# Performance work log

Measured on AMD Instinct MI355X. Metric: run time of the kernel, lower is better.

Reference implementation:

```python
import jax, jax.numpy as jnp
import numpy as np
import math

N_HEAD = 16
D_MODEL = 1024
ATT_DIM = D_MODEL // N_HEAD


def setup_inputs() -> dict:
    key = jax.random.key(0)
    ks = jax.random.split(key, 11)
    B, T, D = 2, 2048, D_MODEL
    s = 1.0 / math.sqrt(D)
    return {
        "q": jax.random.normal(ks[0], (B, T, D), jnp.float32),
        "k": jax.random.normal(ks[1], (B, T, D), jnp.float32),
        "v": jax.random.normal(ks[2], (B, T, D), jnp.float32),
        "Wq": jax.random.normal(ks[3], (D, D), jnp.float32) * s,
        "bq": jnp.zeros((D,), jnp.float32),
        "Wk": jax.random.normal(ks[4], (D, D), jnp.float32) * s,
        "bk": jnp.zeros((D,), jnp.float32),
        "Wv": jax.random.normal(ks[5], (D, D), jnp.float32) * s,
        "bv": jnp.zeros((D,), jnp.float32),
        "Wo": jax.random.normal(ks[6], (D, D), jnp.float32) * s,
        "bo": jnp.zeros((D,), jnp.float32),
    }


def reference(q, k, v, Wq, bq, Wk, bk, Wv, bv, Wo, bo):
    B, T, D = q.shape
    H, hd = N_HEAD, ATT_DIM
    # Linear projections (torch Linear: x @ W.T + b)
    qh = (q @ Wq.T + bq).reshape(B, T, H, hd).transpose(0, 2, 1, 3)  # [B,H,T,hd]
    kh = (k @ Wk.T + bk).reshape(B, T, H, hd).transpose(0, 2, 1, 3)
    vh = (v @ Wv.T + bv).reshape(B, T, H, hd).transpose(0, 2, 1, 3)
    scale = 1.0 / math.sqrt(hd)
    score = jnp.einsum("bhqd,bhkd->bhqk", qh, kh) * scale  # [B,H,T,T]
    attn = jax.nn.softmax(score, axis=-1)
    out = jnp.einsum("bhqk,bhkd->bhqd", attn, vh)  # [B,H,T,hd]
    out = out.transpose(0, 2, 1, 3).reshape(B, T, D)
    return out @ Wo.T + bo
```

## Files before the change

kernel.cpp:

```cpp
#include <hip/hip_runtime.h>


typedef __attribute__((ext_vector_type(8))) short bf16x8;
typedef __attribute__((ext_vector_type(4))) float f32x4;

#define E22 ((size_t)1 << 22)
#define E20 ((size_t)1 << 20)

__device__ __forceinline__ unsigned short f2bf(float x) {
    unsigned int u = __float_as_uint(x);
    u += 0x7fffu + ((u >> 16) & 1u);
    return (unsigned short)(u >> 16);
}
__device__ __forceinline__ unsigned int pk2bf(float a, float b) {
    return __builtin_amdgcn_perm(__float_as_uint(a), __float_as_uint(b), 0x03020706u);
}
__device__ __forceinline__ void gl16(const void* g, void* l) {
    __builtin_amdgcn_global_load_lds(
        (const __attribute__((address_space(1))) void*)g,
        (__attribute__((address_space(3))) void*)l, 16, 0, 0);
}
__device__ __forceinline__ f32x4 mfma16(bf16x8 a, bf16x8 b, f32x4 c) {
    return __builtin_amdgcn_mfma_f32_16x16x32_bf16(a, b, c, 0, 0, 0);
}

__global__ __launch_bounds__(256)
void split_all(const float* __restrict__ q, const float* __restrict__ k,
               const float* __restrict__ v, const float* __restrict__ wq,
               const float* __restrict__ wk, const float* __restrict__ wv,
               const float* __restrict__ wo, unsigned short* __restrict__ ws)
{
    const size_t t = (size_t)blockIdx.x * 256 + threadIdx.x;
    const size_t e = t * 4;
    const float* src; unsigned short* dst; size_t off;
    if (e < 3 * E22) {
        const unsigned int which = (unsigned int)(e >> 22);
        src = which == 0 ? q : (which == 1 ? k : v);
        off = e & (E22 - 1);
        dst = ws + (size_t)which * E22;
    } else {
        const size_t e2 = e - 3 * E22;
        const unsigned int which = (unsigned int)(e2 >> 20);
        off = e2 & (E20 - 1);
        src = which == 0 ? wq : (which == 1 ? wk : (which == 2 ? wv : wo));
        dst = ws + 3 * E22 + (size_t)which * E20;
    }
    const float4 xv = *(const float4*)(src + off);
    ushort4 h4;
    h4.x = f2bf(xv.x); h4.y = f2bf(xv.y); h4.z = f2bf(xv.z); h4.w = f2bf(xv.w);
    *(ushort4*)(dst + off) = h4;
}

__global__ __launch_bounds__(256)
void gemm_qkv(const unsigned short* __restrict__ Xall,
              const unsigned short* __restrict__ Wcat,
              const float* __restrict__ bq, const float* __restrict__ bk,
              const float* __restrict__ bv, unsigned short* __restrict__ Qhp,
              unsigned short* __restrict__ Khp, unsigned short* __restrict__ Vtp)
{
    __shared__ unsigned short Xs[4096], Ws[4096];
    const int tid = threadIdx.x;
    const int w = tid >> 6, ln = tid & 63;
    const int quad = ln >> 4, L = ln & 15;
    const int wy = w >> 1, wx = w & 1;

    const int bid = blockIdx.x;
    const int xcd = bid & 7, j = bid >> 3;
    const int gg = xcd * 12 + (j >> 3);
    const int which = gg >> 5, m_i = gg & 31, n_i = j & 7;
    const int m0 = m_i * 128;

    const unsigned short* X = Xall + (size_t)which * E22;
    const unsigned short* W = Wcat + ((size_t)which * 1024 + n_i * 128) * 1024;
    const float* bp = which == 0 ? bq : (which == 1 ? bk : bv);
    unsigned short* outp = which == 0 ? Qhp : (which == 1 ? Khp : Vtp);
    const float qscale = which == 0 ? 0.18033688011f : 1.0f;

    f32x4 acc[4][4];
#pragma unroll
    for (int i = 0; i < 4; ++i)
#pragma unroll
        for (int jj = 0; jj < 4; ++jj) { f32x4 z = {0.f,0.f,0.f,0.f}; acc[i][jj] = z; }

    for (int k0 = 0; k0 < 1024; k0 += 32) {
        __syncthreads();
#pragma unroll
        for (int i = 0; i < 2; ++i) {
            const int ci  = i * 64 + ln;
            const int row = w * 32 + (ci >> 2);
            const int gc  = (ci & 3) ^ ((row >> 1) & 3);
            const size_t goff = (size_t)row * 1024 + k0 + gc * 8;
            const int lb = w * 2048 + i * 1024;
            gl16(X + (size_t)m0 * 1024 + goff, (char*)Xs + lb);
            gl16(W + goff, (char*)Ws + lb);
        }
        __syncthreads();

        bf16x8 ah[4], bh[4];
#pragma unroll
        for (int mt = 0; mt < 4; ++mt) {
            const int row = wy * 64 + mt * 16 + L;
            ah[mt] = *(const bf16x8*)(Xs + row * 32 + ((quad ^ ((row >> 1) & 3)) * 8));
        }
#pragma unroll
        for (int nt = 0; nt < 4; ++nt) {
            const int row = wx * 64 + nt * 16 + L;
            bh[nt] = *(const bf16x8*)(Ws + row * 32 + ((quad ^ ((row >> 1) & 3)) * 8));
        }
#pragma unroll
        for (int mt = 0; mt < 4; ++mt)
#pragma unroll
            for (int nt = 0; nt < 4; ++nt)
                acc[mt][nt] = mfma16(ah[mt], bh[nt], acc[mt][nt]);
    }

#pragma unroll
    for (int mt = 0; mt < 4; ++mt)
#pragma unroll
        for (int nt = 0; nt < 4; ++nt) {
            const int gm0 = m0 + wy * 64 + mt * 16 + quad * 4;
            const int bn  = n_i * 128 + wx * 64 + nt * 16 + L;
            const float bvv = bp[bn];
            const int hh = bn >> 6, dd = bn & 63;
            if (which < 2) {
#pragma unroll
                for (int r = 0; r < 4; ++r) {
                    const int gm = gm0 + r;
                    const int bb = gm >> 11, tt = gm & 2047;
                    outp[((size_t)(bb * 16 + hh) * 2048 + tt) * 64 + dd] =
                        f2bf((acc[mt][nt][r] + bvv) * qscale);
                }
            } else {
                const int bb = gm0 >> 11, t0 = gm0 & 2047;
                ushort4 pk;
                pk.x = f2bf(acc[mt][nt][0] + bvv);
                pk.y = f2bf(acc[mt][nt][1] + bvv);
                pk.z = f2bf(acc[mt][nt][2] + bvv);
                pk.w = f2bf(acc[mt][nt][3] + bvv);
                *(ushort4*)(outp + ((size_t)(bb * 16 + hh) * 64 + dd) * 2048 + t0) = pk;
            }
        }
}

__global__ __launch_bounds__(256)
void gemm_out(const unsigned short* __restrict__ X, const unsigned short* __restrict__ W,
              const float* __restrict__ bias, float* __restrict__ outp)
{
    __shared__ unsigned short Xs[4096], Ws[2048];
    const int tid = threadIdx.x;
    const int w = tid >> 6, ln = tid & 63;
    const int quad = ln >> 4, L = ln & 15;

    const int bid = blockIdx.x;
    const int xcd = bid & 7, j = bid >> 3;
    const int m0 = (xcd * 4 + (j >> 4)) * 128;
    const int n0 = (j & 15) * 64;

    f32x4 acc[2][4];
#pragma unroll
    for (int i = 0; i < 2; ++i)
#pragma unroll
        for (int jj = 0; jj < 4; ++jj) { f32x4 z = {0.f,0.f,0.f,0.f}; acc[i][jj] = z; }

    for (int k0 = 0; k0 < 1024; k0 += 32) {
        __syncthreads();
#pragma unroll
        for (int i = 0; i < 2; ++i) {
            const int ci  = i * 64 + ln;
            const int row = w * 32 + (ci >> 2);
            const int gc  = (ci & 3) ^ ((row >> 1) & 3);
            const size_t gx = (size_t)(m0 + row) * 1024 + k0 + gc * 8;
            gl16(X + gx, (char*)Xs + w * 2048 + i * 1024);
        }
        {
            const int row = w * 16 + (ln >> 2);
            const int gc  = (ln & 3) ^ ((row >> 1) & 3);
            const size_t gw = (size_t)(n0 + row) * 1024 + k0 + gc * 8;
            gl16(W + gw, (char*)Ws + w * 1024);
        }
        __syncthreads();

        bf16x8 ah[2], bh[4];
#pragma unroll
        for (int mt = 0; mt < 2; ++mt) {
            const int row = w * 32 + mt * 16 + L;
            ah[mt] = *(const bf16x8*)(Xs + row * 32 + ((quad ^ ((row >> 1) & 3)) * 8));
        }
#pragma unroll
        for (int nt = 0; nt < 4; ++nt) {
            const int row = nt * 16 + L;
            bh[nt] = *(const bf16x8*)(Ws + row * 32 + ((quad ^ ((row >> 1) & 3)) * 8));
        }
#pragma unroll
        for (int mt = 0; mt < 2; ++mt)
#pragma unroll
            for (int nt = 0; nt < 4; ++nt)
                acc[mt][nt] = mfma16(ah[mt], bh[nt], acc[mt][nt]);
    }

#pragma unroll
    for (int mt = 0; mt < 2; ++mt)
#pragma unroll
        for (int nt = 0; nt < 4; ++nt) {
            const int gm0 = m0 + w * 32 + mt * 16 + quad * 4;
            const int gn  = n0 + nt * 16 + L;
            const float bvv = bias[gn];
#pragma unroll
            for (int r = 0; r < 4; ++r)
                outp[(size_t)(gm0 + r) * 1024 + gn] = acc[mt][nt][r] + bvv;
        }
}

__global__ __launch_bounds__(256, 2)
void flash(const unsigned short* __restrict__ Qh, const unsigned short* __restrict__ Kh,
           const unsigned short* __restrict__ Vt, unsigned short* __restrict__ A)
{
    __shared__ unsigned short KVs[16384];
    __shared__ unsigned short PT[4 * 64 * 72];
    const int tid = threadIdx.x;
    const int w = tid >> 6, ln = tid & 63;
    const int quad = ln >> 4, L = ln & 15;
    const int wq = w & 1, wk = w >> 1;

    const int bid = blockIdx.x;
    const int xcd = bid & 7, j = bid >> 3;
    const int bh_i = xcd * 4 + (j & 3);
    const int qt = j >> 2;
    const int b = bh_i >> 4, h = bh_i & 15;

    const unsigned short* Qb = Qh + ((size_t)bh_i * 2048 + qt * 128 + wq * 64) * 64;
    const unsigned short* Kb = Kh + (size_t)bh_i * 2048 * 64;
    const unsigned short* Vb = Vt + (size_t)bh_i * 64 * 2048;

    bf16x8 bq[4][2];
#pragma unroll
    for (int nt = 0; nt < 4; ++nt)
#pragma unroll
        for (int kc = 0; kc < 2; ++kc)
            bq[nt][kc] = *(const bf16x8*)(Qb + (nt * 16 + L) * 64 + kc * 32 + quad * 8);

    const short one_bf = (short)0x3F80;
    bf16x8 bone = {one_bf, one_bf, one_bf, one_bf, one_bf, one_bf, one_bf, one_bf};

    f32x4 o[4][4];
    f32x4 lacc[4];
#pragma unroll
    for (int mtd = 0; mtd < 4; ++mtd)
#pragma unroll
        for (int nt = 0; nt < 4; ++nt) { f32x4 z = {0.f,0.f,0.f,0.f}; o[mtd][nt] = z; }
#pragma unroll
    for (int nt = 0; nt < 4; ++nt) { f32x4 z = {0.f,0.f,0.f,0.f}; lacc[nt] = z; }

    unsigned short* Pw = PT + w * 64 * 72;

    const int ci0 = (w * 2 + 0) * 64 + ln, ci1 = (w * 2 + 1) * 64 + ln;
    const int rr0 = ci0 >> 3, rr1 = ci1 >> 3;
    const int gc0 = (ci0 & 7) ^ (rr0 & 7), gc1 = (ci1 & 7) ^ (rr1 & 7);

#define STAGE(kt_, buf_)                                                        \
    do {                                                                        \
        gl16(Kb + (size_t)((kt_) * 64 + rr0) * 64 + gc0 * 8,                    \
             (char*)KVs + (buf_) * 8192 + (w * 2 + 0) * 1024);                  \
        gl16(Kb + (size_t)((kt_) * 64 + rr1) * 64 + gc1 * 8,                    \
             (char*)KVs + (buf_) * 8192 + (w * 2 + 1) * 1024);                  \
        gl16(Vb + (size_t)rr0 * 2048 + (kt_) * 64 + gc0 * 8,                    \
             (char*)KVs + 16384 + (buf_) * 8192 + (w * 2 + 0) * 1024);          \
        gl16(Vb + (size_t)rr1 * 2048 + (kt_) * 64 + gc1 * 8,                    \
             (char*)KVs + 16384 + (buf_) * 8192 + (w * 2 + 1) * 1024);          \
    } while (0)

    STAGE(0, 0);

    for (int kt = 0; kt < 32; ++kt) {
        const int cur = kt & 1;
        __syncthreads();
        if (kt < 31) STAGE(kt + 1, cur ^ 1);

        const unsigned short* Ksb = KVs + cur * 4096;
        const unsigned short* Vsb = KVs + 8192 + cur * 4096;

        bf16x8 ak[2][2];
#pragma unroll
        for (int mt = 0; mt < 2; ++mt)
#pragma unroll
            for (int kc = 0; kc < 2; ++kc) {
                const int row = wk * 32 + mt * 16 + L;
                ak[mt][kc] = *(const bf16x8*)(Ksb + row * 64 + (((kc * 4 + quad) ^ (L & 7)) * 8));
            }

        f32x4 s[2][4];
#pragma unroll
        for (int mt = 0; mt < 2; ++mt)
#pragma unroll
            for (int nt = 0; nt < 4; ++nt) {
                f32x4 z = {0.f,0.f,0.f,0.f};
                z = mfma16(ak[mt][0], bq[nt][0], z);
                z = mfma16(ak[mt][1], bq[nt][1], z);
                s[mt][nt] = z;
            }

#pragma unroll
        for (int mt = 0; mt < 2; ++mt)
#pragma unroll
            for (int nt = 0; nt < 4; ++nt) {
                const float p0 = __builtin_amdgcn_exp2f(s[mt][nt][0]);
                const float p1 = __builtin_amdgcn_exp2f(s[mt][nt][1]);
                const float p2 = __builtin_amdgcn_exp2f(s[mt][nt][2]);
                const float p3 = __builtin_amdgcn_exp2f(s[mt][nt][3]);
                uint2 pk2;
                pk2.x = pk2bf(p0, p1);
                pk2.y = pk2bf(p2, p3);
                *(uint2*)(Pw + (nt * 16 + L) * 72 + mt * 16 + quad * 4) = pk2;
            }
        asm volatile("s_waitcnt lgkmcnt(0)" ::: "memory");

        bf16x8 av[4], pb[4];
#pragma unroll
        for (int mtd = 0; mtd < 4; ++mtd) {
            const int row = mtd * 16 + L;
            av[mtd] = *(const bf16x8*)(Vsb + row * 64 + (((wk * 4 + quad) ^ (L & 7)) * 8));
        }
#pragma unroll
        for (int nt = 0; nt < 4; ++nt)
            pb[nt] = *(const bf16x8*)(Pw + (nt * 16 + L) * 72 + quad * 8);

#pragma unroll
        for (int mtd = 0; mtd < 4; ++mtd)
#pragma unroll
            for (int nt = 0; nt < 4; ++nt)
                o[mtd][nt] = mfma16(av[mtd], pb[nt], o[mtd][nt]);
#pragma unroll
        for (int nt = 0; nt < 4; ++nt)
            lacc[nt] = mfma16(bone, pb[nt], lacc[nt]);
    }
#undef STAGE

    __syncthreads();
    float* Rb = (float*)KVs;
    float* Lb = (float*)PT;
    if (wk == 1) {
#pragma unroll
        for (int mtd = 0; mtd < 4; ++mtd)
#pragma unroll
            for (int nt = 0; nt < 4; ++nt)
                *(f32x4*)(Rb + wq * 4096 + (mtd * 4 + nt) * 256 + ln * 4) = o[mtd][nt];
#pragma unroll
        for (int nt = 0; nt < 4; ++nt)
            *(f32x4*)(Lb + wq * 1024 + nt * 256 + ln * 4) = lacc[nt];
    }
    __syncthreads();
    if (wk == 0) {
#pragma unroll
        for (int mtd = 0; mtd < 4; ++mtd)
#pragma unroll
            for (int nt = 0; nt < 4; ++nt)
                o[mtd][nt] += *(const f32x4*)(Rb + wq * 4096 + (mtd * 4 + nt) * 256 + ln * 4);
#pragma unroll
        for (int nt = 0; nt < 4; ++nt)
            lacc[nt] += *(const f32x4*)(Lb + wq * 1024 + nt * 256 + ln * 4);

#pragma unroll
        for (int nt = 0; nt < 4; ++nt) {
            const float inv = 1.0f / lacc[nt][0];
            const int qrow = b * 2048 + qt * 128 + wq * 64 + nt * 16 + L;
#pragma unroll
            for (int mtd = 0; mtd < 4; ++mtd) {
                const int d0 = mtd * 16 + quad * 4;
                ushort4 pk;
                pk.x = f2bf(o[mtd][nt][0] * inv);
                pk.y = f2bf(o[mtd][nt][1] * inv);
                pk.z = f2bf(o[mtd][nt][2] * inv);
                pk.w = f2bf(o[mtd][nt][3] * inv);
                *(ushort4*)(A + (size_t)qrow * 1024 + h * 64 + d0) = pk;
            }
        }
    }
}

extern "C" void kernel_launch(void* const* d_in, const int* in_sizes, int n_in,
                              void* d_out, int out_size, void* d_ws, size_t ws_size,
                              hipStream_t stream) {
    const float* q  = (const float*)d_in[0];
    const float* k  = (const float*)d_in[1];
    const float* v  = (const float*)d_in[2];
    const float* Wq = (const float*)d_in[3];
    const float* bq = (const float*)d_in[4];
    const float* Wk = (const float*)d_in[5];
    const float* bk = (const float*)d_in[6];
    const float* Wv = (const float*)d_in[7];
    const float* bv = (const float*)d_in[8];
    const float* Wo = (const float*)d_in[9];
    const float* bo = (const float*)d_in[10];

    unsigned short* W = (unsigned short*)d_ws;
    unsigned short *Xall = W;
    unsigned short *Wcat = W + 3 * E22;
    unsigned short *Wob  = Wcat + 3 * E20;
    unsigned short *Qhp  = W + 4 * E22;
    unsigned short *Khp  = W + 5 * E22;
    unsigned short *Vtp  = W + 6 * E22;
    unsigned short *A    = W;

    split_all<<<16384, 256, 0, stream>>>(q, k, v, Wq, Wk, Wv, Wo, W);

    gemm_qkv<<<768, 256, 0, stream>>>(Xall, Wcat, bq, bk, bv, Qhp, Khp, Vtp);

    flash<<<512, 256, 0, stream>>>(Qhp, Khp, Vtp, A);

    gemm_out<<<512, 256, 0, stream>>>(A, Wob, bo, (float*)d_out);
}
```

Baseline: 225.5 us.

## Triple-buffer LDS loads in QKV and output projection GEMMs

Both projection GEMMs now use a three-stage shared-memory ring. Global-to-LDS loads for tile k+2 are issued before the MFMA work on tile k, and a single barrier per iteration, gated by a vmcnt wait, replaces the previous two. The aim is to hide global load latency behind matrix math and cut synchronisation stalls. The cost is three times the LDS per block, which may reduce occupancy, plus hand-counted vmcnt values that must match the number of loads issued.

```diff
diff --git a/kernel.cpp b/kernel.cpp
--- a/kernel.cpp
+++ b/kernel.cpp
@@ -58,7 +58,7 @@
               const float* __restrict__ bv, unsigned short* __restrict__ Qhp,
               unsigned short* __restrict__ Khp, unsigned short* __restrict__ Vtp)
 {
-    __shared__ unsigned short Xs[4096], Ws[4096];
+    __shared__ unsigned short Xs[3 * 4096], Ws[3 * 4096];
     const int tid = threadIdx.x;
     const int w = tid >> 6, ln = tid & 63;
     const int quad = ln >> 4, L = ln & 15;
@@ -76,43 +76,74 @@
     unsigned short* outp = which == 0 ? Qhp : (which == 1 ? Khp : Vtp);
     const float qscale = which == 0 ? 0.18033688011f : 1.0f;
 
+    const int ci0 = ln, ci1 = 64 + ln;
+    const int row0 = w * 32 + (ci0 >> 2), row1 = w * 32 + (ci1 >> 2);
+    const int gc0 = (ci0 & 3) ^ ((row0 >> 1) & 3);
+    const int gc1 = (ci1 & 3) ^ ((row1 >> 1) & 3);
+    const int lb0 = w * 2048, lb1 = w * 2048 + 1024;
+    const unsigned short* Xbp = X + (size_t)m0 * 1024;
+    const size_t gx0 = (size_t)row0 * 1024 + gc0 * 8;
+    const size_t gx1 = (size_t)row1 * 1024 + gc1 * 8;
+
     f32x4 acc[4][4];
 #pragma unroll
     for (int i = 0; i < 4; ++i)
 #pragma unroll
         for (int jj = 0; jj < 4; ++jj) { f32x4 z = {0.f,0.f,0.f,0.f}; acc[i][jj] = z; }
 
-    for (int k0 = 0; k0 < 1024; k0 += 32) {
-        __syncthreads();
-#pragma unroll
-        for (int i = 0; i < 2; ++i) {
-            const int ci  = i * 64 + ln;
-            const int row = w * 32 + (ci >> 2);
-            const int gc  = (ci & 3) ^ ((row >> 1) & 3);
-            const size_t goff = (size_t)row * 1024 + k0 + gc * 8;
-            const int lb = w * 2048 + i * 1024;
-            gl16(X + (size_t)m0 * 1024 + goff, (char*)Xs + lb);
-            gl16(W + goff, (char*)Ws + lb);
-        }
-        __syncthreads();
-
-        bf16x8 ah[4], bh[4];
-#pragma unroll
-        for (int mt = 0; mt < 4; ++mt) {
-            const int row = wy * 64 + mt * 16 + L;
-            ah[mt] = *(const bf16x8*)(Xs + row * 32 + ((quad ^ ((row >> 1) & 3)) * 8));
-        }
-#pragma unroll
-        for (int nt = 0; nt < 4; ++nt) {
-            const int row = wx * 64 + nt * 16 + L;
-            bh[nt] = *(const bf16x8*)(Ws + row * 32 + ((quad ^ ((row >> 1) & 3)) * 8));
-        }
-#pragma unroll
-        for (int mt = 0; mt < 4; ++mt)
-#pragma unroll
-            for (int nt = 0; nt < 4; ++nt)
-                acc[mt][nt] = mfma16(ah[mt], bh[nt], acc[mt][nt]);
-    }
+#define QSTAGE(k0_, bo_)                                                       \
+    do {                                                                       \
+        gl16(Xbp + gx0 + (k0_), (char*)Xs + (bo_) + lb0);                      \
+        gl16(W   + gx0 + (k0_), (char*)Ws + (bo_) + lb0);                      \
+        gl16(Xbp + gx1 + (k0_), (char*)Xs + (bo_) + lb1);                      \
+        gl16(W   + gx1 + (k0_), (char*)Ws + (bo_) + lb1);                      \
+    } while (0)
+
+#define QCOMP(eo_)                                                             \
+    do {                                                                       \
+        const unsigned short* Xc = Xs + (eo_);                                 \
+        const unsigned short* Wc = Ws + (eo_);                                 \
+        bf16x8 ah[4], bh[4];                                                   \
+        _Pragma("unroll")                                                      \
+        for (int mt = 0; mt < 4; ++mt) {                                       \
+            const int row = wy * 64 + mt * 16 + L;                             \
+            ah[mt] = *(const bf16x8*)(Xc + row * 32 +                          \
+                                      ((quad ^ ((row >> 1) & 3)) * 8));        \
+        }                                                                      \
+        _Pragma("unroll")                                                      \
+        for (int nt = 0; nt < 4; ++nt) {                                       \
+            const int row = wx * 64 + nt * 16 + L;                             \
+            bh[nt] = *(const bf16x8*)(Wc + row * 32 +                          \
+                                      ((quad ^ ((row >> 1) & 3)) * 8));        \
+        }                                                                      \
+        _Pragma("unroll")                                                      \
+        for (int mt = 0; mt < 4; ++mt)                                         \
+            _Pragma("unroll")                                                  \
+            for (int nt = 0; nt < 4; ++nt)                                     \
+                acc[mt][nt] = mfma16(ah[mt], bh[nt], acc[mt][nt]);             \
+    } while (0)
+
+    QSTAGE(0, 0);
+    QSTAGE(32, 8192);
+
+    int cur = 0;
+    for (int kt = 0; kt < 31; ++kt) {
+        asm volatile("s_waitcnt vmcnt(4)" ::: "memory");
+        __builtin_amdgcn_s_barrier();
+        asm volatile("" ::: "memory");
+        if (kt < 30) {
+            int st = cur + 2; if (st >= 3) st -= 3;
+            QSTAGE((kt + 2) * 32, st * 8192);
+        }
+        QCOMP(cur * 4096);
+        cur = (cur == 2) ? 0 : cur + 1;
+    }
+    asm volatile("s_waitcnt vmcnt(0)" ::: "memory");
+    __builtin_amdgcn_s_barrier();
+    asm volatile("" ::: "memory");
+    QCOMP(cur * 4096);
+#undef QSTAGE
+#undef QCOMP
 
 #pragma unroll
     for (int mt = 0; mt < 4; ++mt)
@@ -146,7 +177,7 @@
 void gemm_out(const unsigned short* __restrict__ X, const unsigned short* __restrict__ W,
               const float* __restrict__ bias, float* __restrict__ outp)
 {
-    __shared__ unsigned short Xs[4096], Ws[2048];
+    __shared__ unsigned short Xs[3 * 4096], Ws[3 * 2048];
     const int tid = threadIdx.x;
     const int w = tid >> 6, ln = tid & 63;
     const int quad = ln >> 4, L = ln & 15;
@@ -156,47 +187,74 @@
     const int m0 = (xcd * 4 + (j >> 4)) * 128;
     const int n0 = (j & 15) * 64;
 
+    const int cix0 = ln, cix1 = 64 + ln;
+    const int rowx0 = w * 32 + (cix0 >> 2), rowx1 = w * 32 + (cix1 >> 2);
+    const int gcx0 = (cix0 & 3) ^ ((rowx0 >> 1) & 3);
+    const int gcx1 = (cix1 & 3) ^ ((rowx1 >> 1) & 3);
+    const int roww = w * 16 + (ln >> 2);
+    const int gcw = (ln & 3) ^ ((roww >> 1) & 3);
+    const size_t gxx0 = (size_t)(m0 + rowx0) * 1024 + gcx0 * 8;
+    const size_t gxx1 = (size_t)(m0 + rowx1) * 1024 + gcx1 * 8;
+    const size_t gww  = (size_t)(n0 + roww) * 1024 + gcw * 8;
+
     f32x4 acc[2][4];
 #pragma unroll
     for (int i = 0; i < 2; ++i)
 #pragma unroll
         for (int jj = 0; jj < 4; ++jj) { f32x4 z = {0.f,0.f,0.f,0.f}; acc[i][jj] = z; }
 
-    for (int k0 = 0; k0 < 1024; k0 += 32) {
-        __syncthreads();
-#pragma unroll
-        for (int i = 0; i < 2; ++i) {
-            const int ci  = i * 64 + ln;
-            const int row = w * 32 + (ci >> 2);
-            const int gc  = (ci & 3) ^ ((row >> 1) & 3);
-            const size_t gx = (size_t)(m0 + row) * 1024 + k0 + gc * 8;
-            gl16(X + gx, (char*)Xs + w * 2048 + i * 1024);
-        }
-        {
-            const int row = w * 16 + (ln >> 2);
-            const int gc  = (ln & 3) ^ ((row >> 1) & 3);
-            const size_t gw = (size_t)(n0 + row) * 1024 + k0 + gc * 8;
-            gl16(W + gw, (char*)Ws + w * 1024);
-        }
-        __syncthreads();
-
-        bf16x8 ah[2], bh[4];
-#pragma unroll
-        for (int mt = 0; mt < 2; ++mt) {
-            const int row = w * 32 + mt * 16 + L;
-            ah[mt] = *(const bf16x8*)(Xs + row * 32 + ((quad ^ ((row >> 1) & 3)) * 8));
-        }
-#pragma unroll
-        for (int nt = 0; nt < 4; ++nt) {
-            const int row = nt * 16 + L;
-            bh[nt] = *(const bf16x8*)(Ws + row * 32 + ((quad ^ ((row >> 1) & 3)) * 8));
-        }
-#pragma unroll
-        for (int mt = 0; mt < 2; ++mt)
-#pragma unroll
-            for (int nt = 0; nt < 4; ++nt)
-                acc[mt][nt] = mfma16(ah[mt], bh[nt], acc[mt][nt]);
-    }
+#define OSTAGE(k0_, bf_)                                                       \
+    do {                                                                       \
+        gl16(X + gxx0 + (k0_), (char*)Xs + (bf_) * 8192 + w * 2048);           \
+        gl16(X + gxx1 + (k0_), (char*)Xs + (bf_) * 8192 + w * 2048 + 1024);    \
+        gl16(W + gww  + (k0_), (char*)Ws + (bf_) * 4096 + w * 1024);           \
+    } while (0)
+
+#define OCOMP(bf_)                                                             \
+    do {                                                                       \
+        const unsigned short* Xc = Xs + (bf_) * 4096;                          \
+        const unsigned short* Wc = Ws + (bf_) * 2048;                          \
+        bf16x8 ah[2], bh[4];                                                   \
+        _Pragma("unroll")                                                      \
+        for (int mt = 0; mt < 2; ++mt) {                                       \
+            const int row = w * 32 + mt * 16 + L;                              \
+            ah[mt] = *(const bf16x8*)(Xc + row * 32 +                          \
+                                      ((quad ^ ((row >> 1) & 3)) * 8));        \
+        }                                                                      \
+        _Pragma("unroll")                                                      \
+        for (int nt = 0; nt < 4; ++nt) {                                       \
+            const int row = nt * 16 + L;                                       \
+            bh[nt] = *(const bf16x8*)(Wc + row * 32 +                          \
+                                      ((quad ^ ((row >> 1) & 3)) * 8));        \
+        }                                                                      \
+        _Pragma("unroll")                                                      \
+        for (int mt = 0; mt < 2; ++mt)                                         \
+            _Pragma("unroll")                                                  \
+            for (int nt = 0; nt < 4; ++nt)                                     \
+                acc[mt][nt] = mfma16(ah[mt], bh[nt], acc[mt][nt]);             \
+    } while (0)
+
+    OSTAGE(0, 0);
+    OSTAGE(32, 1);
+
+    int cur = 0;
+    for (int kt = 0; kt < 31; ++kt) {
+        asm volatile("s_waitcnt vmcnt(3)" ::: "memory");
+        __builtin_amdgcn_s_barrier();
+        asm volatile("" ::: "memory");
+        if (kt < 30) {
+            int st = cur + 2; if (st >= 3) st -= 3;
+            OSTAGE((kt + 2) * 32, st);
+        }
+        OCOMP(cur);
+        cur = (cur == 2) ? 0 : cur + 1;
+    }
+    asm volatile("s_waitcnt vmcnt(0)" ::: "memory");
+    __builtin_amdgcn_s_barrier();
+    asm volatile("" ::: "memory");
+    OCOMP(cur);
+#undef OSTAGE
+#undef OCOMP
 
 #pragma unroll
     for (int mt = 0; mt < 2; ++mt)
```

Result: faster. 215.6 us (-4.4%).
